# Performance work log

Measured on AMD Instinct MI355X. Metric: run time of the kernel, lower is better.

The kernel has to match this reference:

```python
import jax, jax.numpy as jnp
import numpy as np

ANCHORS = np.array([116., 90., 156., 198., 373., 326.], np.float32).reshape(1, 1, 1, 3, 2)
IGNORE_THRESH = 0.5
OBJ_SCALE = 5.0
NOOBJ_SCALE = 1.0
XYWH_SCALE = 1.0
CLASS_SCALE = 1.0
GRID_SCALE = 1.0


def setup_inputs() -> dict:
    key = jax.random.key(0)
    k1, k2, k3 = jax.random.split(key, 3)
    B, GH, GW, NET, T, C = 16, 64, 64, 1024, 100, 80
    input_image = jnp.zeros((B, NET, NET, 3), jnp.float32)  # only shape is used
    y_pred = jax.random.normal(k1, (B, GH, GW, 3 * (5 + C)), jnp.float32)
    y_true = jax.random.uniform(k2, (B, GH, GW, 3, 5 + C), jnp.float32)
    true_boxes = jax.random.uniform(k3, (B, 1, 1, 1, T, 4), jnp.float32)
    return {"input_image": input_image, "y_pred": y_pred, "y_true": y_true, "true_boxes": true_boxes}


def reference(input_image, y_pred, y_true, true_boxes):
    B, GH, GW = y_true.shape[:3]
    net_h, net_w = input_image.shape[1], input_image.shape[2]
    dtype = y_pred.dtype
    anchors = jnp.asarray(ANCHORS, dtype)  # [1,1,1,3,2]
    y_pred = y_pred.reshape(B, GH, GW, 3, -1)
    object_mask = y_true[..., 4:5]  # [B,GH,GW,3,1]
    grid_factor = jnp.array([GW, GH], dtype).reshape(1, 1, 1, 1, 2)
    net_factor = jnp.array([net_w, net_h], dtype).reshape(1, 1, 1, 1, 2)
    cx, cy = jnp.meshgrid(jnp.arange(GW, dtype=dtype), jnp.arange(GH, dtype=dtype))
    cell_grid = jnp.stack([cx, cy], -1)[None, :, :, None, :]  # [1,GH,GW,1,2]

    # adjust predictions
    pred_box_xy = cell_grid + jax.nn.sigmoid(y_pred[..., :2])
    pred_box_wh = y_pred[..., 2:4]
    pred_box_conf = jax.nn.sigmoid(y_pred[..., 4:5])
    pred_box_class = y_pred[..., 5:]

    # adjust ground truth
    true_box_xy = y_true[..., 0:2]
    true_box_wh = y_true[..., 2:4]
    true_box_class = jnp.argmax(y_true[..., 5:], axis=-1)  # [B,GH,GW,3]

    # broadcast IoU: each predicted box vs all true boxes
    true_xy = true_boxes[..., 0:2] / grid_factor  # [B,1,1,1,T,2]
    true_wh = true_boxes[..., 2:4] / net_factor
    true_half = true_wh / 2.0
    true_mins, true_maxes = true_xy - true_half, true_xy + true_half
    pred_xy = (pred_box_xy / grid_factor)[..., None, :]  # [B,GH,GW,3,1,2]
    pred_wh = (jnp.exp(pred_box_wh) * anchors / net_factor)[..., None, :]
    pred_half = pred_wh / 2.0
    pred_mins, pred_maxes = pred_xy - pred_half, pred_xy + pred_half
    inter_wh = jnp.maximum(jnp.minimum(pred_maxes, true_maxes) - jnp.maximum(pred_mins, true_mins), 0.0)
    inter_area = inter_wh[..., 0] * inter_wh[..., 1]  # [B,GH,GW,3,T]
    true_area = true_wh[..., 0] * true_wh[..., 1]
    pred_area = pred_wh[..., 0] * pred_wh[..., 1]
    iou = inter_area / (pred_area + true_area - inter_area)
    best_ious = jnp.max(iou, axis=4)
    conf_ignore_mask = (best_ious > IGNORE_THRESH).astype(dtype)[..., None]

    # post-warmup branch (batch_seen > warmup_batches)
    xywh_mask = object_mask

    wh_scale = jnp.exp(true_box_wh) * anchors / net_factor
    wh_scale = (2.0 - wh_scale[..., 0] * wh_scale[..., 1])[..., None]

    xy_delta = xywh_mask * (true_box_xy - pred_box_xy) * wh_scale * XYWH_SCALE
    wh_delta = xywh_mask * (true_box_wh - pred_box_wh) * wh_scale * XYWH_SCALE
    conf_delta = (0.0 - pred_box_conf) * NOOBJ_SCALE
    conf_delta = conf_delta + object_mask * (1.0 - pred_box_conf) * OBJ_SCALE
    conf_delta = conf_delta * (1.0 - (1.0 - object_mask) * conf_ignore_mask)
    log_p = jax.nn.log_softmax(pred_box_class, axis=-1)
    ce = -jnp.take_along_axis(log_p, true_box_class[..., None], axis=-1)  # [B,GH,GW,3,1]
    class_delta = object_mask * ce * CLASS_SCALE

    delta = jnp.concatenate([xy_delta, wh_delta, conf_delta, class_delta], axis=-1)  # [B,GH,GW,3,6]
    loss = jnp.sum(jnp.square(delta), axis=(1, 2, 3, 4))
    return loss * GRID_SCALE
```

## Files before the change

### kernel.cpp

```cpp
#include <hip/hip_runtime.h>


#define NT 100
#define CPB 12288
#define NTOT 196608

typedef float f4 __attribute__((ext_vector_type(4)));
typedef f4 f4a __attribute__((aligned(4)));

__device__ __forceinline__ float frcp(float x) { return __builtin_amdgcn_rcpf(x); }
__device__ __forceinline__ float fsig(float x) { return frcp(1.f + __expf(-x)); }

__global__ __launch_bounds__(256, 2) void yolo_loss_kernel(
    const float* __restrict__ y_pred,
    const float* __restrict__ y_true,
    const float* __restrict__ true_boxes,
    float* __restrict__ out)
{
    __shared__ f4 sbox[NT];
    __shared__ float swsum[4];

    const int tid = threadIdx.x;
    const int gth = blockIdx.x * 256 + tid;
    const int row = gth >> 1;
    const int q   = gth & 1;
    const int b   = row / CPB;

    if (tid < NT) {
        const f4 tb = *(const f4*)(true_boxes + (size_t)b * NT * 4 + tid * 4);
        const float tx = tb.x * (1.f / 64.f),   ty = tb.y * (1.f / 64.f);
        const float tw = tb.z * (1.f / 1024.f), th = tb.w * (1.f / 1024.f);
        f4 r;
        r.x = tx - 0.5f * tw; r.y = ty - 0.5f * th;
        r.z = tx + 0.5f * tw; r.w = ty + 0.5f * th;
        sbox[tid] = r;
    }
    __syncthreads();

    const int rem = row % CPB;
    const int gy  = rem / 192;
    const int rr  = rem - gy * 192;
    const int gx  = rr / 3;
    const int a   = rr - gx * 3;
    const float aw = (a == 0) ? 116.f : ((a == 1) ? 156.f : 373.f);
    const float ah = (a == 0) ? 90.f  : ((a == 1) ? 198.f : 326.f);

    const float* p = y_pred + (size_t)row * 85;
    const float* t = y_true + (size_t)row * 85;

    const f4 ph = *(const f4a*)p;   const float p4v = p[4];
    const f4 th = *(const f4a*)t;   const float om  = t[4];

    const f4a* pc4 = (const f4a*)(p + 5 + 40 * q);
    const f4a* tc4 = (const f4a*)(t + 5 + 40 * q);

    float ssum = 0.f;
    float tmax = -1e30f, psel = 0.f;

    f4 pa0 = pc4[0], pa1 = pc4[1], ta0 = tc4[0], ta1 = tc4[1];
#pragma unroll
    for (int bch = 0; bch < 5; ++bch) {
        const f4 pb0 = pa0, pb1 = pa1, tb0 = ta0, tb1 = ta1;
        if (bch < 4) {
            pa0 = pc4[2 * bch + 2]; pa1 = pc4[2 * bch + 3];
            ta0 = tc4[2 * bch + 2]; ta1 = tc4[2 * bch + 3];
        }
#pragma unroll
        for (int c = 0; c < 4; ++c) {
            float pv = pb0[c], tv = tb0[c];
            ssum += __expf(pv);
            bool g = tv > tmax;
            tmax = g ? tv : tmax; psel = g ? pv : psel;
            pv = pb1[c]; tv = tb1[c];
            ssum += __expf(pv);
            g = tv > tmax;
            tmax = g ? tv : tmax; psel = g ? pv : psel;
        }
    }
    ssum += __shfl_xor(ssum, 1, 64);
    const float otmax = __shfl_xor(tmax, 1, 64);
    const float opsel = __shfl_xor(psel, 1, 64);
    const bool adopt = (otmax > tmax) || (otmax == tmax && q == 1);
    psel = adopt ? opsel : psel;
    const float ce = __logf(ssum) - psel;

    const float predx = (float)gx + fsig(ph.x);
    const float predy = (float)gy + fsig(ph.y);
    const float conf  = fsig(p4v);
    const float pw  = __expf(ph.z) * aw * (1.f / 1024.f);
    const float phh = __expf(ph.w) * ah * (1.f / 1024.f);
    const float parea = pw * phh;
    const float px = predx * (1.f / 64.f), py = predy * (1.f / 64.f);
    const float pminx = px - 0.5f * pw,  pmaxx = px + 0.5f * pw;
    const float pminy = py - 0.5f * phh, pmaxy = py + 0.5f * phh;

    float best = 0.f;
#pragma unroll 5
    for (int ti = q; ti < NT; ti += 2) {
        const f4 bx = sbox[ti];
        float iw = fminf(pmaxx, bx.z) - fmaxf(pminx, bx.x);
        float ih = fminf(pmaxy, bx.w) - fmaxf(pminy, bx.y);
        iw = fmaxf(iw, 0.f); ih = fmaxf(ih, 0.f);
        const float inter = iw * ih;
        const float tarea = (bx.z - bx.x) * (bx.w - bx.y);
        best = fmaxf(best, inter * frcp(parea + tarea - inter));
    }
    best = fmaxf(best, __shfl_xor(best, 1, 64));
    const float ignore = (best > 0.5f) ? 1.f : 0.f;

    const float wsx = __expf(th.z) * aw * (1.f / 1024.f);
    const float wsy = __expf(th.w) * ah * (1.f / 1024.f);
    const float ws  = 2.f - wsx * wsy;
    const float omws = om * ws;
    const float dx = omws * (th.x - predx);
    const float dy = omws * (th.y - predy);
    const float dw = omws * (th.z - ph.z);
    const float dh = omws * (th.w - ph.w);
    float dc = -conf + om * (1.f - conf) * 5.f;
    dc *= (1.f - (1.f - om) * ignore);
    const float dcl = om * ce;

    float val = dx * dx + dy * dy + dw * dw + dh * dh + dc * dc + dcl * dcl;
    val = (q == 0) ? val : 0.f;

#pragma unroll
    for (int off = 32; off > 0; off >>= 1) val += __shfl_down(val, off, 64);
    if ((tid & 63) == 0) swsum[tid >> 6] = val;
    __syncthreads();
    if (tid == 0) atomicAdd(out + b, swsum[0] + swsum[1] + swsum[2] + swsum[3]);
}

extern "C" void kernel_launch(void* const* d_in, const int* in_sizes, int n_in,
                              void* d_out, int out_size, void* d_ws, size_t ws_size,
                              hipStream_t stream) {
    const float* y_pred     = (const float*)d_in[1];
    const float* y_true     = (const float*)d_in[2];
    const float* true_boxes = (const float*)d_in[3];
    float* out = (float*)d_out;

    hipMemsetAsync(d_out, 0, (size_t)out_size * sizeof(float), stream);
    yolo_loss_kernel<<<(NTOT * 2) / 256, 256, 0, stream>>>(y_pred, y_true, true_boxes, out);
}
```

Baseline: 328.3 us.

## Split each anchor row across four lanes with interleaved f4 loads

Each 85-float anchor row is now handled by four lanes instead of two. The lanes load interleaved 16-byte groups, so neighbouring lanes touch adjacent memory, and the class argmax/logsumexp and IoU max are combined with a 4-lane shuffle reduction that breaks ties by class index. The change aims to improve coalescing and raise the thread count per row for this bandwidth-bound kernel. In exchange it adds more redundant per-row header math, more shuffles, and a launch with twice as many blocks; the occupancy hint on launch bounds is also dropped.

```diff
diff --git a/kernel.cpp b/kernel.cpp
--- a/kernel.cpp
+++ b/kernel.cpp
@@ -4,6 +4,7 @@
 #define NT 100
 #define CPB 12288
 #define NTOT 196608
+#define ROWS_PER_BLOCK 64
 
 typedef float f4 __attribute__((ext_vector_type(4)));
 typedef f4 f4a __attribute__((aligned(4)));
@@ -11,7 +12,7 @@
 __device__ __forceinline__ float frcp(float x) { return __builtin_amdgcn_rcpf(x); }
 __device__ __forceinline__ float fsig(float x) { return frcp(1.f + __expf(-x)); }
 
-__global__ __launch_bounds__(256, 2) void yolo_loss_kernel(
+__global__ __launch_bounds__(256) void yolo_loss_kernel(
     const float* __restrict__ y_pred,
     const float* __restrict__ y_true,
     const float* __restrict__ true_boxes,
@@ -21,9 +22,8 @@
     __shared__ float swsum[4];
 
     const int tid = threadIdx.x;
-    const int gth = blockIdx.x * 256 + tid;
-    const int row = gth >> 1;
-    const int q   = gth & 1;
+    const int q   = tid & 3;
+    const int row = blockIdx.x * ROWS_PER_BLOCK + (tid >> 2);
     const int b   = row / CPB;
 
     if (tid < NT) {
@@ -48,47 +48,71 @@
     const float* p = y_pred + (size_t)row * 85;
     const float* t = y_true + (size_t)row * 85;
 
-    const f4 ph = *(const f4a*)p;   const float p4v = p[4];
-    const f4 th = *(const f4a*)t;   const float om  = t[4];
+    const f4 g0 = *(const f4a*)p;
+    const f4 g1 = *(const f4a*)(p + 4);
+    const f4 h0 = *(const f4a*)t;
+    const f4 h1 = *(const f4a*)(t + 4);
 
-    const f4a* pc4 = (const f4a*)(p + 5 + 40 * q);
-    const f4a* tc4 = (const f4a*)(t + 5 + 40 * q);
+    const int ng = (q == 3) ? 4 : 5;
+    f4 pg[5], tg[5];
+#pragma unroll
+    for (int k = 0; k < 5; ++k) {
+        const int j  = 2 + q + 4 * k;
+        const int jj = (j <= 20) ? j : 5;
+        pg[k] = *(const f4a*)(p + 4 * jj);
+        tg[k] = *(const f4a*)(t + 4 * jj);
+    }
+    float ptail = 0.f, ttail = 0.f;
+    if (q == 3) { ptail = p[84]; ttail = t[84]; }
 
-    float ssum = 0.f;
-    float tmax = -1e30f, psel = 0.f;
+    const float p4v = g1.x, om = h1.x;
 
-    f4 pa0 = pc4[0], pa1 = pc4[1], ta0 = tc4[0], ta1 = tc4[1];
+    float ssum = 0.f, tmax = -1e30f, psel = 0.f;
+    int jm = 1 << 20;
+    if (q == 0) {
 #pragma unroll
-    for (int bch = 0; bch < 5; ++bch) {
-        const f4 pb0 = pa0, pb1 = pa1, tb0 = ta0, tb1 = ta1;
-        if (bch < 4) {
-            pa0 = pc4[2 * bch + 2]; pa1 = pc4[2 * bch + 3];
-            ta0 = tc4[2 * bch + 2]; ta1 = tc4[2 * bch + 3];
-        }
-#pragma unroll
-        for (int c = 0; c < 4; ++c) {
-            float pv = pb0[c], tv = tb0[c];
+        for (int e = 1; e < 4; ++e) {
+            const float pv = g1[e], tv = h1[e];
             ssum += __expf(pv);
-            bool g = tv > tmax;
-            tmax = g ? tv : tmax; psel = g ? pv : psel;
-            pv = pb1[c]; tv = tb1[c];
-            ssum += __expf(pv);
-            g = tv > tmax;
-            tmax = g ? tv : tmax; psel = g ? pv : psel;
+            const bool g = tv > tmax;
+            tmax = g ? tv : tmax; psel = g ? pv : psel; jm = g ? (e - 1) : jm;
         }
     }
-    ssum += __shfl_xor(ssum, 1, 64);
-    const float otmax = __shfl_xor(tmax, 1, 64);
-    const float opsel = __shfl_xor(psel, 1, 64);
-    const bool adopt = (otmax > tmax) || (otmax == tmax && q == 1);
-    psel = adopt ? opsel : psel;
+#pragma unroll
+    for (int k = 0; k < 5; ++k) {
+        if (k < ng) {
+            const int j = 2 + q + 4 * k;
+#pragma unroll
+            for (int e = 0; e < 4; ++e) {
+                const float pv = pg[k][e], tv = tg[k][e];
+                ssum += __expf(pv);
+                const bool g = tv > tmax;
+                tmax = g ? tv : tmax; psel = g ? pv : psel;
+                jm = g ? (4 * j + e - 5) : jm;
+            }
+        }
+    }
+    if (q == 3) {
+        ssum += __expf(ptail);
+        const bool g = ttail > tmax;
+        tmax = g ? ttail : tmax; psel = g ? ptail : psel; jm = g ? 79 : jm;
+    }
+#pragma unroll
+    for (int off = 1; off < 4; off <<= 1) {
+        ssum += __shfl_xor(ssum, off, 64);
+        const float otm = __shfl_xor(tmax, off, 64);
+        const float ops = __shfl_xor(psel, off, 64);
+        const int   ojm = __shfl_xor(jm, off, 64);
+        const bool adopt = (otm > tmax) || (otm == tmax && ojm < jm);
+        tmax = adopt ? otm : tmax; psel = adopt ? ops : psel; jm = adopt ? ojm : jm;
+    }
     const float ce = __logf(ssum) - psel;
 
-    const float predx = (float)gx + fsig(ph.x);
-    const float predy = (float)gy + fsig(ph.y);
+    const float predx = (float)gx + fsig(g0.x);
+    const float predy = (float)gy + fsig(g0.y);
     const float conf  = fsig(p4v);
-    const float pw  = __expf(ph.z) * aw * (1.f / 1024.f);
-    const float phh = __expf(ph.w) * ah * (1.f / 1024.f);
+    const float pw  = __expf(g0.z) * aw * (1.f / 1024.f);
+    const float phh = __expf(g0.w) * ah * (1.f / 1024.f);
     const float parea = pw * phh;
     const float px = predx * (1.f / 64.f), py = predy * (1.f / 64.f);
     const float pminx = px - 0.5f * pw,  pmaxx = px + 0.5f * pw;
@@ -96,8 +120,8 @@
 
     float best = 0.f;
 #pragma unroll 5
-    for (int ti = q; ti < NT; ti += 2) {
-        const f4 bx = sbox[ti];
+    for (int k = 0; k < 25; ++k) {
+        const f4 bx = sbox[q + 4 * k];
         float iw = fminf(pmaxx, bx.z) - fmaxf(pminx, bx.x);
         float ih = fminf(pmaxy, bx.w) - fmaxf(pminy, bx.y);
         iw = fmaxf(iw, 0.f); ih = fmaxf(ih, 0.f);
@@ -105,17 +129,19 @@
         const float tarea = (bx.z - bx.x) * (bx.w - bx.y);
         best = fmaxf(best, inter * frcp(parea + tarea - inter));
     }
-    best = fmaxf(best, __shfl_xor(best, 1, 64));
+#pragma unroll
+    for (int off = 1; off < 4; off <<= 1)
+        best = fmaxf(best, __shfl_xor(best, off, 64));
     const float ignore = (best > 0.5f) ? 1.f : 0.f;
 
-    const float wsx = __expf(th.z) * aw * (1.f / 1024.f);
-    const float wsy = __expf(th.w) * ah * (1.f / 1024.f);
+    const float wsx = __expf(h0.z) * aw * (1.f / 1024.f);
+    const float wsy = __expf(h0.w) * ah * (1.f / 1024.f);
     const float ws  = 2.f - wsx * wsy;
     const float omws = om * ws;
-    const float dx = omws * (th.x - predx);
-    const float dy = omws * (th.y - predy);
-    const float dw = omws * (th.z - ph.z);
-    const float dh = omws * (th.w - ph.w);
+    const float dx = omws * (h0.x - predx);
+    const float dy = omws * (h0.y - predy);
+    const float dw = omws * (h0.z - g0.z);
+    const float dh = omws * (h0.w - g0.w);
     float dc = -conf + om * (1.f - conf) * 5.f;
     dc *= (1.f - (1.f - om) * ignore);
     const float dcl = om * ce;
@@ -139,5 +165,5 @@
     float* out = (float*)d_out;
 
     hipMemsetAsync(d_out, 0, (size_t)out_size * sizeof(float), stream);
-    yolo_loss_kernel<<<(NTOT * 2) / 256, 256, 0, stream>>>(y_pred, y_true, true_boxes, out);
+    yolo_loss_kernel<<<NTOT / ROWS_PER_BLOCK, 256, 0, stream>>>(y_pred, y_true, true_boxes, out);
 }
```

Measured after the change: 314.5 us. 1.04x faster.
